# Optimization experiments

Hardware: AMD Instinct MI355X
Metric: run time of the kernel (lower is better)

The kernel has to match this reference:

```python
import jax, jax.numpy as jnp
import numpy as np

B, NV, NS, L = 32, 2048, 512, 64
FEAT, SEM, HID, ATT, DM = 1024, 512, 512, 512, 512


def setup_inputs() -> dict:
    key = jax.random.key(0)
    ks = jax.random.split(key, 14)
    s = lambda k, sh: jax.random.normal(k, sh, dtype=jnp.float32) * 0.02
    return {
        "query": jax.random.normal(ks[0], (B, 1, HID), dtype=jnp.float32),
        "visual_features": jax.random.normal(ks[1], (B, NV, FEAT), dtype=jnp.float32),
        "semantic_features": jax.random.normal(ks[2], (B, NS, SEM), dtype=jnp.float32),
        "patient_info": jax.random.normal(ks[3], (B, L, DM), dtype=jnp.float32),
        "W1v": s(ks[4], (HID, ATT)),
        "W2v": s(ks[5], (FEAT, ATT)),
        "vv": s(ks[6], (ATT, 1)),
        "W3": s(ks[7], (DM, ATT)),
        "b3": jnp.zeros((ATT,), dtype=jnp.float32),
        "W1s": s(ks[8], (HID, ATT)),
        "W2s": s(ks[9], (SEM, ATT)),
        "vs": s(ks[10], (ATT, 1)),
        "W": s(ks[11], (FEAT + SEM, FEAT)),
        "bW": jnp.zeros((FEAT,), dtype=jnp.float32),
    }


def reference(query, visual_features, semantic_features, patient_info,
              W1v, W2v, vv, W3, b3, W1s, W2s, vs, W, bW):
    # mean over patient sequence, project: [B,1,ATT]
    pinfo = jnp.mean(patient_info, axis=1, keepdims=True) @ W3 + b3
    q_v = query @ W1v          # [B,1,ATT]
    # visual branch
    v_scores = jnp.tanh(q_v + visual_features @ W2v + pinfo) @ vv  # [B,NV,1]
    v_attn = jax.nn.softmax(v_scores, axis=1)
    # semantic branch
    q_s = query @ W1s
    s_scores = jnp.tanh(q_s + semantic_features @ W2s + pinfo) @ vs  # [B,NS,1]
    s_attn = jax.nn.softmax(s_scores, axis=1)
    ctx = jnp.concatenate([
        jnp.sum(visual_features * v_attn, axis=1),    # [B,FEAT]
        jnp.sum(semantic_features * s_attn, axis=1),  # [B,SEM]
    ], axis=1) @ W + bW
    return ctx, v_attn, s_attn
```

## Files before the change

kernel.cpp:

```cpp
#include <hip/hip_runtime.h>

typedef float f32x4 __attribute__((ext_vector_type(4)));
typedef short short8 __attribute__((ext_vector_type(8)));

#define B_    32
#define NV_   2048
#define NS_   512
#define L_    64
#define FEAT_ 1024
#define SEM_  512
#define HID_  512
#define ATT_  512
#define DM_   512

__device__ __forceinline__ unsigned int f2bf_pk(float lo, float hi) {
  unsigned int ul = (__float_as_uint(lo) + 0x8000u) >> 16;
  unsigned int uh = (__float_as_uint(hi) + 0x8000u) & 0xffff0000u;
  return uh | ul;
}

__device__ __forceinline__ unsigned short f2bf(float f) {
  return (unsigned short)((__float_as_uint(f) + 0x8000u) >> 16);
}

__device__ __forceinline__ float bflo(unsigned int u) { return __uint_as_float(u << 16); }
__device__ __forceinline__ float bfhi(unsigned int u) { return __uint_as_float(u & 0xffff0000u); }

__device__ __forceinline__ float fast_tanh(float x) {
  float e = __expf(2.f * x);
  return 1.f - 2.f * __builtin_amdgcn_rcpf(e + 1.f);
}

__global__ __launch_bounds__(256) void k_pmean(const float* __restrict__ pat,
                                               float* __restrict__ pm) {
  int b = blockIdx.x, t = threadIdx.x;
  for (int d = t; d < DM_; d += 256) {
    float s = 0.f;
    for (int l = 0; l < L_; ++l) s += pat[(b * L_ + l) * DM_ + d];
    pm[b * DM_ + d] = s * (1.f / 64.f);
  }
}

__global__ __launch_bounds__(256) void k_qp(const float* __restrict__ query,
                                            const float* __restrict__ pm,
                                            const float* __restrict__ W1v,
                                            const float* __restrict__ W1s,
                                            const float* __restrict__ W3,
                                            const float* __restrict__ b3,
                                            float* __restrict__ qpv,
                                            float* __restrict__ qps) {
  int idx = blockIdx.x * 256 + threadIdx.x;
  int b = idx >> 9, a = idx & 511;
  float pi = b3[a];
  for (int d = 0; d < DM_; ++d) pi += pm[b * DM_ + d] * W3[d * ATT_ + a];
  float qv = 0.f, qs = 0.f;
  for (int h = 0; h < HID_; ++h) {
    float q = query[b * HID_ + h];
    qv += q * W1v[h * ATT_ + a];
    qs += q * W1s[h * ATT_ + a];
  }
  qpv[idx] = qv + pi;
  qps[idx] = qs + pi;
}

__global__ __launch_bounds__(256) void k_swz(const float* __restrict__ W2,
                                             unsigned short* __restrict__ out,
                                             int total) {
  int idx = blockIdx.x * 256 + threadIdx.x;
  if (idx >= total) return;
  int k = idx >> 9, c = idx & 511;
  int kc = k >> 5, kr = k & 31, q = kr >> 3, j = kr & 7;
  int cb = c >> 4, n = c & 15;
  out[(kc * 32 + cb) * 512 + q * 128 + n * 8 + j] = f2bf(W2[idx]);
}

__global__ __launch_bounds__(256, 2) void k_scores_fused(
    const float* __restrict__ X, const unsigned short* __restrict__ Wt,
    const float* __restrict__ qp, const float* __restrict__ vvec,
    float* __restrict__ score, unsigned short* __restrict__ Av,
    int K, int rows_per_batch) {
  __shared__ __align__(16) unsigned short As[2048];
  const int t = threadIdx.x;
  const int lane = t & 63, wave = t >> 6;
  const int quad = lane >> 4, l15 = lane & 15;
  const int row0 = blockIdx.x * 64;
  const int b = row0 / rows_per_batch;
  const int nk = K >> 5;
  const int rt128 = blockIdx.x >> 1;
  const int rbOff = (blockIdx.x & 1) * 4;

  const int r = t >> 2, q_ = t & 3;
  const int arb = r >> 4, am = r & 15;
  const float* gA = X + (size_t)(row0 + r) * K + q_ * 8;
  uint4* asDst = (uint4*)(As + arb * 512 + q_ * 128 + am * 8);
  char* avBase = (char*)(Av + (size_t)rt128 * nk * 4096) +
                 (rbOff + arb) * 1024 + q_ * 256 + am * 16;

  const char* gB = (const char*)Wt + (size_t)wave * 8192 + lane * 16;

  const f32x4 zero = {0.f, 0.f, 0.f, 0.f};
  f32x4 acc[4][8];
#pragma unroll
  for (int a = 0; a < 4; ++a)
#pragma unroll
    for (int cb = 0; cb < 8; ++cb) acc[a][cb] = zero;

  for (int kc = 0; kc < nk; ++kc) {
    short8 bfr[8];
    const char* gBk = gB + (size_t)kc * 32768;
#pragma unroll
    for (int cb = 0; cb < 8; ++cb)
      bfr[cb] = *(const short8*)(gBk + cb * 1024);

    __syncthreads();
    const float4 v0 = *(const float4*)(gA + kc * 32);
    const float4 v1 = *(const float4*)(gA + kc * 32 + 4);
    uint4 o;
    o.x = f2bf_pk(v0.x, v0.y);
    o.y = f2bf_pk(v0.z, v0.w);
    o.z = f2bf_pk(v1.x, v1.y);
    o.w = f2bf_pk(v1.z, v1.w);
    *asDst = o;
    *(uint4*)(avBase + (size_t)kc * 8192) = o;
    __syncthreads();

    short8 af[4];
#pragma unroll
    for (int a = 0; a < 4; ++a)
      af[a] = *(const short8*)(As + a * 512 + quad * 128 + l15 * 8);
#pragma unroll
    for (int a = 0; a < 4; ++a)
#pragma unroll
      for (int cb = 0; cb < 8; ++cb)
        acc[a][cb] = __builtin_amdgcn_mfma_f32_16x16x32_bf16(af[a], bfr[cb], acc[a][cb], 0, 0, 0);
  }

  float qv_[8], vw_[8];
#pragma unroll
  for (int cb = 0; cb < 8; ++cb) {
    int col = wave * 128 + cb * 16 + l15;
    qv_[cb] = qp[b * ATT_ + col];
    vw_[cb] = vvec[col];
  }
#pragma unroll
  for (int a = 0; a < 4; ++a) {
#pragma unroll
    for (int rr = 0; rr < 4; ++rr) {
      float s = 0.f;
#pragma unroll
      for (int cb = 0; cb < 8; ++cb)
        s += fast_tanh(acc[a][cb][rr] + qv_[cb]) * vw_[cb];
      s += __shfl_xor(s, 1);
      s += __shfl_xor(s, 2);
      s += __shfl_xor(s, 4);
      s += __shfl_xor(s, 8);
      if (l15 == 0) atomicAdd(&score[row0 + a * 16 + quad * 4 + rr], s);
    }
  }
}

__global__ __launch_bounds__(256) void k_scores_f32(const float* __restrict__ X,
                                                    const unsigned short* __restrict__ Wt,
                                                    const float* __restrict__ qp,
                                                    const float* __restrict__ vvec,
                                                    float* __restrict__ score,
                                                    int K, int rows_per_batch) {
  __shared__ __align__(16) unsigned short As[4096];
  __shared__ __align__(16) unsigned short Bs[4096];
  const int t = threadIdx.x;
  const int lane = t & 63;
  const int wave = t >> 6;
  const int wr = wave & 1, wc = wave >> 1;
  const int quad = lane >> 4, l15 = lane & 15;
  const int row0 = blockIdx.x * 128;
  const int ct = blockIdx.y;
  const int b = row0 / rows_per_batch;

  const int ai_row = t >> 3;
  const int ai_k0 = (t & 7) * 4;
  const int a_q = ai_k0 >> 3;
  const int a_j0 = ai_k0 & 7;

  const f32x4 zero = {0.f, 0.f, 0.f, 0.f};
  f32x4 acc[4][4];
#pragma unroll
  for (int a = 0; a < 4; ++a)
#pragma unroll
    for (int bb = 0; bb < 4; ++bb) acc[a][bb] = zero;

  const int nk = K >> 5;
  for (int kc = 0; kc < nk; ++kc) {
    __syncthreads();
#pragma unroll
    for (int ii = 0; ii < 4; ++ii) {
      int i = ii * 32 + ai_row;
      const float4 v = *(const float4*)(X + (size_t)(row0 + i) * K + kc * 32 + ai_k0);
      uint2 h;
      h.x = f2bf_pk(v.x, v.y);
      h.y = f2bf_pk(v.z, v.w);
      int rb = i >> 4, m = i & 15;
      *(uint2*)(As + rb * 512 + a_q * 128 + m * 8 + a_j0) = h;
    }
    {
      const uint4* src = (const uint4*)(Wt + (size_t)(kc * 32 + ct * 8) * 512);
      uint4* dst = (uint4*)Bs;
      dst[t] = src[t];
      dst[t + 256] = src[t + 256];
    }
    __syncthreads();
    short8 af[4], bfr[4];
#pragma unroll
    for (int a = 0; a < 4; ++a)
      af[a] = *(const short8*)(As + (wr * 4 + a) * 512 + quad * 128 + l15 * 8);
#pragma unroll
    for (int bb = 0; bb < 4; ++bb)
      bfr[bb] = *(const short8*)(Bs + (wc * 4 + bb) * 512 + quad * 128 + l15 * 8);
#pragma unroll
    for (int a = 0; a < 4; ++a)
#pragma unroll
      for (int bb = 0; bb < 4; ++bb)
        acc[a][bb] = __builtin_amdgcn_mfma_f32_16x16x32_bf16(af[a], bfr[bb], acc[a][bb], 0, 0, 0);
  }

  const int colbase = ct * 128 + wc * 64;
  float qv_[4], vw_[4];
#pragma unroll
  for (int bb = 0; bb < 4; ++bb) {
    int col = colbase + bb * 16 + l15;
    qv_[bb] = qp[b * ATT_ + col];
    vw_[bb] = vvec[col];
  }
#pragma unroll
  for (int a = 0; a < 4; ++a) {
#pragma unroll
    for (int r = 0; r < 4; ++r) {
      float s = 0.f;
#pragma unroll
      for (int bb = 0; bb < 4; ++bb)
        s += fast_tanh(acc[a][bb][r] + qv_[bb]) * vw_[bb];
      s += __shfl_xor(s, 1);
      s += __shfl_xor(s, 2);
      s += __shfl_xor(s, 4);
      s += __shfl_xor(s, 8);
      if (l15 == 0) {
        int row = row0 + wr * 64 + a * 16 + quad * 4 + r;
        atomicAdd(&score[row], s);
      }
    }
  }
}

__global__ __launch_bounds__(256) void k_softmax(const float* __restrict__ score,
                                                 float* __restrict__ attn, int N) {
  __shared__ float sm[4];
  int b = blockIdx.x, t = threadIdx.x;
  const float* s = score + (size_t)b * N;
  float m = -1e30f;
  for (int i = t; i < N; i += 256) m = fmaxf(m, s[i]);
  for (int k = 32; k; k >>= 1) m = fmaxf(m, __shfl_xor(m, k));
  if ((t & 63) == 0) sm[t >> 6] = m;
  __syncthreads();
  m = fmaxf(fmaxf(sm[0], sm[1]), fmaxf(sm[2], sm[3]));
  __syncthreads();
  float sum = 0.f;
  for (int i = t; i < N; i += 256) sum += __expf(s[i] - m);
  for (int k = 32; k; k >>= 1) sum += __shfl_xor(sum, k);
  if ((t & 63) == 0) sm[t >> 6] = sum;
  __syncthreads();
  sum = sm[0] + sm[1] + sm[2] + sm[3];
  float inv = 1.f / sum;
  for (int i = t; i < N; i += 256) attn[(size_t)b * N + i] = __expf(s[i] - m) * inv;
}

__global__ __launch_bounds__(256) void k_wsum_swz(const unsigned short* __restrict__ Aswz,
                                                  const float* __restrict__ attn,
                                                  float* __restrict__ ctx_pre,
                                                  int nkc, int rtPerBatch,
                                                  int rowsPerBatch, int colOff) {
  const int b = blockIdx.x, kc = blockIdx.y;
  const int t = threadIdx.x, q = t >> 6, l = t & 63;
  const int rbl = l >> 4, m = l & 15;
  float acc[8] = {0.f, 0.f, 0.f, 0.f, 0.f, 0.f, 0.f, 0.f};
  for (int rt = 0; rt < rtPerBatch; ++rt) {
    const unsigned short* blk = Aswz + ((size_t)(b * rtPerBatch + rt) * nkc + kc) * 4096;
    const float* ab = attn + (size_t)b * rowsPerBatch + rt * 128;
#pragma unroll
    for (int p = 0; p < 2; ++p) {
      int rb = p * 4 + rbl;
      float a = ab[rb * 16 + m];
      uint4 v = *(const uint4*)(blk + rb * 512 + q * 128 + m * 8);
      acc[0] += a * bflo(v.x);
      acc[1] += a * bfhi(v.x);
      acc[2] += a * bflo(v.y);
      acc[3] += a * bfhi(v.y);
      acc[4] += a * bflo(v.z);
      acc[5] += a * bfhi(v.z);
      acc[6] += a * bflo(v.w);
      acc[7] += a * bfhi(v.w);
    }
  }
#pragma unroll
  for (int off = 1; off < 64; off <<= 1) {
#pragma unroll
    for (int j = 0; j < 8; ++j) acc[j] += __shfl_xor(acc[j], off);
  }
  if (l == 0) {
    float* dst = ctx_pre + b * 1536 + colOff + kc * 32 + q * 8;
#pragma unroll
    for (int j = 0; j < 8; ++j) dst[j] = acc[j];
  }
}

__global__ __launch_bounds__(256) void k_wsum(const float* __restrict__ feats,
                                              const float* __restrict__ attn,
                                              float* __restrict__ ctx_pre,
                                              int N, int F, int colOff, int rowsPerChunk) {
  int b = blockIdx.x, rc = blockIdx.y, t = threadIdx.x;
  int c4 = t * 4;
  if (c4 >= F) return;
  int r0 = rc * rowsPerChunk;
  const float* fb = feats + ((size_t)b * N + r0) * F;
  const float* ab = attn + (size_t)b * N + r0;
  float4 acc = {0.f, 0.f, 0.f, 0.f};
  for (int r = 0; r < rowsPerChunk; ++r) {
    float a = ab[r];
    float4 v = *(const float4*)(fb + (size_t)r * F + c4);
    acc.x += a * v.x; acc.y += a * v.y; acc.z += a * v.z; acc.w += a * v.w;
  }
  float* dst = ctx_pre + b * 1536 + colOff + c4;
  atomicAdd(dst + 0, acc.x);
  atomicAdd(dst + 1, acc.y);
  atomicAdd(dst + 2, acc.z);
  atomicAdd(dst + 3, acc.w);
}

__global__ __launch_bounds__(256) void k_final(const float* __restrict__ cp,
                                               const float* __restrict__ W,
                                               const float* __restrict__ bW,
                                               float* __restrict__ out) {
  int b = blockIdx.x, oc = blockIdx.y, t = threadIdx.x;
  int o = oc * 256 + t;
  float acc = bW[o];
  const float* c = cp + b * 1536;
  for (int k = 0; k < 1536; ++k) acc += c[k] * W[k * FEAT_ + o];
  out[b * FEAT_ + o] = acc;
}

extern "C" void kernel_launch(void* const* d_in, const int* in_sizes, int n_in,
                              void* d_out, int out_size, void* d_ws, size_t ws_size,
                              hipStream_t stream) {
  const float* query = (const float*)d_in[0];
  const float* vf    = (const float*)d_in[1];
  const float* sf    = (const float*)d_in[2];
  const float* pat   = (const float*)d_in[3];
  const float* W1v   = (const float*)d_in[4];
  const float* W2v   = (const float*)d_in[5];
  const float* vv    = (const float*)d_in[6];
  const float* W3    = (const float*)d_in[7];
  const float* b3    = (const float*)d_in[8];
  const float* W1s   = (const float*)d_in[9];
  const float* W2s   = (const float*)d_in[10];
  const float* vs    = (const float*)d_in[11];
  const float* W     = (const float*)d_in[12];
  const float* bW    = (const float*)d_in[13];
  float* out = (float*)d_out;

  char* ws = (char*)d_ws;
  float* scores_v = (float*)(ws);
  float* scores_s = (float*)(ws + 262144);
  float* ctx_pre  = (float*)(ws + 327680);
  float* pm   = (float*)(ws + 524288);
  float* qpv  = (float*)(ws + 589824);
  float* qps  = (float*)(ws + 655360);
  unsigned short* Wtv = (unsigned short*)(ws + 720896);
  unsigned short* Wts = (unsigned short*)(ws + 720896 + 1048576);
  unsigned short* Av  = (unsigned short*)(ws + 4194304);
  unsigned short* Asm = (unsigned short*)(ws + 4194304 + 134217728);
  const size_t NEED = 4194304ull + 134217728ull + 16777216ull;
  const bool bf16path = (ws_size >= NEED);

  hipMemsetAsync(d_ws, 0, bf16path ? 327680 : 524288, stream);

  k_pmean<<<32, 256, 0, stream>>>(pat, pm);
  k_qp<<<64, 256, 0, stream>>>(query, pm, W1v, W1s, W3, b3, qpv, qps);
  k_swz<<<(FEAT_ * ATT_) / 256, 256, 0, stream>>>(W2v, Wtv, FEAT_ * ATT_);
  k_swz<<<(SEM_ * ATT_) / 256, 256, 0, stream>>>(W2s, Wts, SEM_ * ATT_);

  float* v_attn = out + B_ * FEAT_;
  float* s_attn = out + B_ * FEAT_ + B_ * NV_;

  if (bf16path) {
    k_scores_fused<<<(B_ * NV_) / 64, 256, 0, stream>>>(vf, Wtv, qpv, vv, scores_v, Av, FEAT_, NV_);
    k_scores_fused<<<(B_ * NS_) / 64, 256, 0, stream>>>(sf, Wts, qps, vs, scores_s, Asm, SEM_, NS_);
    k_softmax<<<B_, 256, 0, stream>>>(scores_v, v_attn, NV_);
    k_softmax<<<B_, 256, 0, stream>>>(scores_s, s_attn, NS_);
    k_wsum_swz<<<dim3(B_, FEAT_ / 32), 256, 0, stream>>>(Av, v_attn, ctx_pre, FEAT_ / 32, NV_ / 128, NV_, 0);
    k_wsum_swz<<<dim3(B_, SEM_ / 32), 256, 0, stream>>>(Asm, s_attn, ctx_pre, SEM_ / 32, NS_ / 128, NS_, 1024);
  } else {
    k_scores_f32<<<dim3((B_ * NV_) / 128, 4), 256, 0, stream>>>(vf, Wtv, qpv, vv, scores_v, FEAT_, NV_);
    k_scores_f32<<<dim3((B_ * NS_) / 128, 4), 256, 0, stream>>>(sf, Wts, qps, vs, scores_s, SEM_, NS_);
    k_softmax<<<B_, 256, 0, stream>>>(scores_v, v_attn, NV_);
    k_softmax<<<B_, 256, 0, stream>>>(scores_s, s_attn, NS_);
    k_wsum<<<dim3(B_, 8), 256, 0, stream>>>(vf, v_attn, ctx_pre, NV_, FEAT_, 0, 256);
    k_wsum<<<dim3(B_, 2), 256, 0, stream>>>(sf, s_attn, ctx_pre, NS_, SEM_, 1024, 256);
  }

  k_final<<<dim3(B_, 4), 256, 0, stream>>>(ctx_pre, W, bW, out);
}
```

Baseline: 685.8 us.

## Double-buffer LDS and prefetch next K-chunk in fused score GEMM

Converts the fused score kernel's main loop into a software pipeline. The LDS A tile is double-buffered and the next iteration's X and W2 fragments are loaded into registers before the current MFMAs run. This cuts one barrier per iteration and hides global-load latency behind compute. The cost is higher register pressure (extra rBn and A registers on top of 128 accumulator floats), which may reduce occupancy under launch_bounds(256,2) or cause spills.

```diff
diff --git a/kernel.cpp b/kernel.cpp
--- a/kernel.cpp
+++ b/kernel.cpp
@@ -79,7 +79,7 @@
     const float* __restrict__ qp, const float* __restrict__ vvec,
     float* __restrict__ score, unsigned short* __restrict__ Av,
     int K, int rows_per_batch) {
-  __shared__ __align__(16) unsigned short As[2048];
+  __shared__ __align__(16) unsigned short As[2][2048];
   const int t = threadIdx.x;
   const int lane = t & 63, wave = t >> 6;
   const int quad = lane >> 4, l15 = lane & 15;
@@ -92,7 +92,7 @@
   const int r = t >> 2, q_ = t & 3;
   const int arb = r >> 4, am = r & 15;
   const float* gA = X + (size_t)(row0 + r) * K + q_ * 8;
-  uint4* asDst = (uint4*)(As + arb * 512 + q_ * 128 + am * 8);
+  const int asOff = arb * 512 + q_ * 128 + am * 8;
   char* avBase = (char*)(Av + (size_t)rt128 * nk * 4096) +
                  (rbOff + arb) * 1024 + q_ * 256 + am * 16;
 
@@ -105,34 +105,49 @@
 #pragma unroll
     for (int cb = 0; cb < 8; ++cb) acc[a][cb] = zero;
 
+  float4 a0 = *(const float4*)(gA);
+  float4 a1 = *(const float4*)(gA + 4);
+  short8 rB[8];
+#pragma unroll
+  for (int cb = 0; cb < 8; ++cb) rB[cb] = *(const short8*)(gB + cb * 1024);
+
+#pragma unroll 2
   for (int kc = 0; kc < nk; ++kc) {
-    short8 bfr[8];
-    const char* gBk = gB + (size_t)kc * 32768;
-#pragma unroll
-    for (int cb = 0; cb < 8; ++cb)
-      bfr[cb] = *(const short8*)(gBk + cb * 1024);
+    uint4 o;
+    o.x = f2bf_pk(a0.x, a0.y);
+    o.y = f2bf_pk(a0.z, a0.w);
+    o.z = f2bf_pk(a1.x, a1.y);
+    o.w = f2bf_pk(a1.z, a1.w);
+    *(uint4*)(&As[kc & 1][asOff]) = o;
+    *(uint4*)(avBase + (size_t)kc * 8192) = o;
+
+    short8 rBn[8];
+    bool more = (kc + 1 < nk);
+    if (more) {
+      const float* gAn = gA + (kc + 1) * 32;
+      a0 = *(const float4*)(gAn);
+      a1 = *(const float4*)(gAn + 4);
+      const char* gBn = gB + (size_t)(kc + 1) * 32768;
+#pragma unroll
+      for (int cb = 0; cb < 8; ++cb) rBn[cb] = *(const short8*)(gBn + cb * 1024);
+    }
 
     __syncthreads();
-    const float4 v0 = *(const float4*)(gA + kc * 32);
-    const float4 v1 = *(const float4*)(gA + kc * 32 + 4);
-    uint4 o;
-    o.x = f2bf_pk(v0.x, v0.y);
-    o.y = f2bf_pk(v0.z, v0.w);
-    o.z = f2bf_pk(v1.x, v1.y);
-    o.w = f2bf_pk(v1.z, v1.w);
-    *asDst = o;
-    *(uint4*)(avBase + (size_t)kc * 8192) = o;
-    __syncthreads();
 
     short8 af[4];
 #pragma unroll
     for (int a = 0; a < 4; ++a)
-      af[a] = *(const short8*)(As + a * 512 + quad * 128 + l15 * 8);
+      af[a] = *(const short8*)(&As[kc & 1][a * 512 + quad * 128 + l15 * 8]);
 #pragma unroll
     for (int a = 0; a < 4; ++a)
 #pragma unroll
       for (int cb = 0; cb < 8; ++cb)
-        acc[a][cb] = __builtin_amdgcn_mfma_f32_16x16x32_bf16(af[a], bfr[cb], acc[a][cb], 0, 0, 0);
+        acc[a][cb] = __builtin_amdgcn_mfma_f32_16x16x32_bf16(af[a], rB[cb], acc[a][cb], 0, 0, 0);
+
+    if (more) {
+#pragma unroll
+      for (int cb = 0; cb < 8; ++cb) rB[cb] = rBn[cb];
+    }
   }
 
   float qv_[8], vw_[8];
```

Result: no change. 691.8 us (+0.9%).
